# Performance work log

Measured on AMD Instinct MI355X. Metric: run time of the kernel, lower is better.

## Reference

```python
import jax, jax.numpy as jnp
import numpy as np

EPS = 1e-8  # matches F.cosine_similarity default eps
SIM_TARGET = 1  # int(self.sim_matrix), a scalar constant


def setup_inputs() -> dict:
    key = jax.random.key(0)
    k1, k2 = jax.random.split(key)
    input1 = jax.random.normal(k1, (4096, 1024), dtype=jnp.float32)  # [U, P]
    input2 = jax.random.normal(k2, (4096, 1024), dtype=jnp.float32)  # [V, P]
    return {"input1": input1, "input2": input2}


def reference(input1, input2):
    # Row-normalize with eps clamp (same as F.cosine_similarity per pair)
    n1 = input1 / jnp.maximum(jnp.linalg.norm(input1, axis=1, keepdims=True), EPS)
    n2 = input2 / jnp.maximum(jnp.linalg.norm(input2, axis=1, keepdims=True), EPS)
    cos = jnp.einsum('up,vp->uv', n1, n2)  # [U, V] pairwise cosine similarity
    return jnp.sum((SIM_TARGET - cos) ** 2)
```

## Files before the change

### kernel.cpp

```cpp
#include <hip/hip_runtime.h>
#include <hip/hip_bf16.h>
#include <stdint.h>

#define U_ROWS 4096
#define P_DIM  1024
#define TM     256
#define TN     128
#define BK     64

typedef float f32x4 __attribute__((ext_vector_type(4)));
typedef long  lx2   __attribute__((ext_vector_type(2)));

__global__ __launch_bounds__(256) void norm_fp8_kernel(
    const float* __restrict__ in1, const float* __restrict__ in2,
    uint8_t* __restrict__ out, float* __restrict__ loss_out) {
    const int w = threadIdx.x >> 6, lane = threadIdx.x & 63;
    const int row = blockIdx.x * 4 + w;
    const float* src = (row < U_ROWS) ? (in1 + (size_t)row * P_DIM)
                                      : (in2 + (size_t)(row - U_ROWS) * P_DIM);
    float4 v[4];
    float ss = 0.0f;
    #pragma unroll
    for (int j = 0; j < 4; ++j) {
        v[j] = ((const float4*)src)[j * 64 + lane];
        ss += v[j].x * v[j].x + v[j].y * v[j].y + v[j].z * v[j].z + v[j].w * v[j].w;
    }
    #pragma unroll
    for (int off = 32; off > 0; off >>= 1) ss += __shfl_xor(ss, off, 64);
    const float inv = 16.0f / fmaxf(sqrtf(ss), 1e-8f);

    uint8_t* orow = out + (size_t)row * P_DIM;
    #pragma unroll
    for (int j = 0; j < 4; ++j) {
        int c = j * 256 + lane * 4;
        int pos = (c & 4) + (((c >> 3) & 3) * 16) + (((c >> 5) & 1) * 8);
        int newc = (c & ~63) | pos;
        int d = __builtin_amdgcn_cvt_pk_fp8_f32(v[j].x * inv, v[j].y * inv, 0, false);
        d = __builtin_amdgcn_cvt_pk_fp8_f32(v[j].z * inv, v[j].w * inv, d, true);
        *(int*)(orow + newc) = d;
    }
    if (blockIdx.x == 0 && threadIdx.x == 0) *loss_out = 0.0f;
}

__global__ __launch_bounds__(512) void cosloss_gemm_fp8(
    const uint8_t* __restrict__ n1, const uint8_t* __restrict__ n2,
    float* __restrict__ loss_out) {
    __shared__ uint8_t As[TM * BK];
    __shared__ uint8_t Bs[TN * BK];
    __shared__ float red[8];

    const int tid  = threadIdx.x;
    const int w    = tid >> 6;
    const int lane = tid & 63;

    const int id  = blockIdx.x;
    const int xcd = id & 7;
    const int j   = id >> 3;
    const int cb  = xcd * 4 + (j & 3);
    const int rb  = j >> 2;

    const uint8_t* gA = n1 + (size_t)rb * TM * P_DIM;
    const uint8_t* gB = n2 + (size_t)cb * TN * P_DIM;

    const int srow = lane >> 2;
    const int scol = (lane & 3) * 16;
    const int chunk0 = w * 3;

    f32x4 acc[4][4];
    #pragma unroll
    for (int mi = 0; mi < 4; ++mi)
        #pragma unroll
        for (int ni = 0; ni < 4; ++ni)
            acc[mi][ni] = (f32x4){0.f, 0.f, 0.f, 0.f};

    const int wr = (w >> 1) * 64;
    const int wc = (w & 1) * 64;
    const int fr = lane & 15;
    const int q  = lane >> 4;

    for (int kt = 0; kt < P_DIM / BK; ++kt) {
        #pragma unroll
        for (int cc = 0; cc < 3; ++cc) {
            const int c = chunk0 + cc;
            const uint8_t* g;
            uint8_t* s;
            if (c < 16) {
                g = gA + (size_t)(c * 16 + srow) * P_DIM + kt * BK + scol;
                s = As + c * 1024;
            } else {
                g = gB + (size_t)((c - 16) * 16 + srow) * P_DIM + kt * BK + scol;
                s = Bs + (c - 16) * 1024;
            }
            __builtin_amdgcn_global_load_lds(
                (const __attribute__((address_space(1))) void*)g,
                (__attribute__((address_space(3))) void*)s,
                16, 0, 0);
        }
        __syncthreads();

        lx2 af[4], bfr[4];
        #pragma unroll
        for (int i = 0; i < 4; ++i) {
            af[i]  = *(const lx2*)(As + (wr + i * 16 + fr) * BK + q * 16);
            bfr[i] = *(const lx2*)(Bs + (wc + i * 16 + fr) * BK + q * 16);
        }
        #pragma unroll
        for (int mi = 0; mi < 4; ++mi)
            #pragma unroll
            for (int ni = 0; ni < 4; ++ni) {
                acc[mi][ni] = __builtin_amdgcn_mfma_f32_16x16x32_fp8_fp8(
                    af[mi].x, bfr[ni].x, acc[mi][ni], 0, 0, 0);
                acc[mi][ni] = __builtin_amdgcn_mfma_f32_16x16x32_fp8_fp8(
                    af[mi].y, bfr[ni].y, acc[mi][ni], 0, 0, 0);
            }
        __syncthreads();
    }

    float local = 0.0f;
    #pragma unroll
    for (int mi = 0; mi < 4; ++mi)
        #pragma unroll
        for (int ni = 0; ni < 4; ++ni)
            #pragma unroll
            for (int r = 0; r < 4; ++r) {
                const float d = 1.0f - acc[mi][ni][r] * (1.0f / 256.0f);
                local += d * d;
            }
    #pragma unroll
    for (int off = 32; off > 0; off >>= 1) local += __shfl_down(local, off, 64);
    if (lane == 0) red[w] = local;
    __syncthreads();
    if (tid == 0) {
        float t = 0.0f;
        #pragma unroll
        for (int i = 0; i < 8; ++i) t += red[i];
        atomicAdd(loss_out, t);
    }
}

extern "C" void kernel_launch(void* const* d_in, const int* in_sizes, int n_in,
                              void* d_out, int out_size, void* d_ws, size_t ws_size,
                              hipStream_t stream) {
    const float* in1 = (const float*)d_in[0];
    const float* in2 = (const float*)d_in[1];
    float* out = (float*)d_out;
    uint8_t* nrm = (uint8_t*)d_ws;

    norm_fp8_kernel<<<(U_ROWS * 2) / 4, 256, 0, stream>>>(in1, in2, nrm, out);

    cosloss_gemm_fp8<<<(U_ROWS / TM) * (U_ROWS / TN), 512, 0, stream>>>(
        nrm, nrm + (size_t)U_ROWS * P_DIM, out);
}
```

Baseline: 101.5 us.

## Switch FP8 GEMM to scaled 16x16x128 MFMA with swizzled K=128 tiles

Replaces the pairs of 16x16x32 fp8 MFMAs with the gfx950 scaled 16x16x128 f8f6f4 MFMA using unit scales, and doubles BK to 128 so each k-step issues one wide MFMA per tile. The normalization kernel now writes each row contiguously with a row-rotated 16-byte swizzle so the GEMM's LDS reads avoid bank conflicts. Launch bounds now request 4 blocks per CU. The aim is higher matrix throughput and fewer instructions and barriers, at the cost of a larger LDS footprint (48KB per block), which may limit occupancy.

```diff
diff --git a/kernel.cpp b/kernel.cpp
--- a/kernel.cpp
+++ b/kernel.cpp
@@ -6,10 +6,11 @@
 #define P_DIM  1024
 #define TM     256
 #define TN     128
-#define BK     64
+#define BK     128
 
 typedef float f32x4 __attribute__((ext_vector_type(4)));
-typedef long  lx2   __attribute__((ext_vector_type(2)));
+typedef int   i32x4 __attribute__((ext_vector_type(4)));
+typedef int   i32x8 __attribute__((ext_vector_type(8)));
 
 __global__ __launch_bounds__(256) void norm_fp8_kernel(
     const float* __restrict__ in1, const float* __restrict__ in2,
@@ -22,27 +23,28 @@
     float ss = 0.0f;
     #pragma unroll
     for (int j = 0; j < 4; ++j) {
-        v[j] = ((const float4*)src)[j * 64 + lane];
+        v[j] = ((const float4*)src)[lane * 4 + j];
         ss += v[j].x * v[j].x + v[j].y * v[j].y + v[j].z * v[j].z + v[j].w * v[j].w;
     }
     #pragma unroll
     for (int off = 32; off > 0; off >>= 1) ss += __shfl_xor(ss, off, 64);
     const float inv = 16.0f / fmaxf(sqrtf(ss), 1e-8f);
 
-    uint8_t* orow = out + (size_t)row * P_DIM;
+    i32x4 d;
     #pragma unroll
     for (int j = 0; j < 4; ++j) {
-        int c = j * 256 + lane * 4;
-        int pos = (c & 4) + (((c >> 3) & 3) * 16) + (((c >> 5) & 1) * 8);
-        int newc = (c & ~63) | pos;
-        int d = __builtin_amdgcn_cvt_pk_fp8_f32(v[j].x * inv, v[j].y * inv, 0, false);
-        d = __builtin_amdgcn_cvt_pk_fp8_f32(v[j].z * inv, v[j].w * inv, d, true);
-        *(int*)(orow + newc) = d;
+        int dj = __builtin_amdgcn_cvt_pk_fp8_f32(v[j].x * inv, v[j].y * inv, 0, false);
+        dj = __builtin_amdgcn_cvt_pk_fp8_f32(v[j].z * inv, v[j].w * inv, dj, true);
+        d[j] = dj;
     }
+    const int blk = lane >> 3;
+    const int gi  = lane & 7;
+    uint8_t* orow = out + (size_t)row * P_DIM;
+    *(i32x4*)(orow + blk * 128 + (((gi + row) & 7) * 16)) = d;
     if (blockIdx.x == 0 && threadIdx.x == 0) *loss_out = 0.0f;
 }
 
-__global__ __launch_bounds__(512) void cosloss_gemm_fp8(
+__global__ __launch_bounds__(512, 4) void cosloss_gemm_mx(
     const uint8_t* __restrict__ n1, const uint8_t* __restrict__ n2,
     float* __restrict__ loss_out) {
     __shared__ uint8_t As[TM * BK];
@@ -62,9 +64,9 @@
     const uint8_t* gA = n1 + (size_t)rb * TM * P_DIM;
     const uint8_t* gB = n2 + (size_t)cb * TN * P_DIM;
 
-    const int srow = lane >> 2;
-    const int scol = (lane & 3) * 16;
-    const int chunk0 = w * 3;
+    const int srow = lane >> 3;
+    const int scol = (lane & 7) * 16;
+    const int c0   = w * 6;
 
     f32x4 acc[4][4];
     #pragma unroll
@@ -80,16 +82,16 @@
 
     for (int kt = 0; kt < P_DIM / BK; ++kt) {
         #pragma unroll
-        for (int cc = 0; cc < 3; ++cc) {
-            const int c = chunk0 + cc;
+        for (int cc = 0; cc < 6; ++cc) {
+            const int c = c0 + cc;
             const uint8_t* g;
             uint8_t* s;
-            if (c < 16) {
-                g = gA + (size_t)(c * 16 + srow) * P_DIM + kt * BK + scol;
+            if (c < 32) {
+                g = gA + (size_t)(c * 8 + srow) * P_DIM + kt * BK + scol;
                 s = As + c * 1024;
             } else {
-                g = gB + (size_t)((c - 16) * 16 + srow) * P_DIM + kt * BK + scol;
-                s = Bs + (c - 16) * 1024;
+                g = gB + (size_t)((c - 32) * 8 + srow) * P_DIM + kt * BK + scol;
+                s = Bs + (c - 32) * 1024;
             }
             __builtin_amdgcn_global_load_lds(
                 (const __attribute__((address_space(1))) void*)g,
@@ -98,21 +100,30 @@
         }
         __syncthreads();
 
-        lx2 af[4], bfr[4];
+        i32x8 af[4];
         #pragma unroll
         for (int i = 0; i < 4; ++i) {
-            af[i]  = *(const lx2*)(As + (wr + i * 16 + fr) * BK + q * 16);
-            bfr[i] = *(const lx2*)(Bs + (wc + i * 16 + fr) * BK + q * 16);
+            const int row = wr + i * 16 + fr;
+            const uint8_t* rbase = As + row * BK;
+            i32x4 lo = *(const i32x4*)(rbase + (((q * 2 + 0 + row) & 7) * 16));
+            i32x4 hi = *(const i32x4*)(rbase + (((q * 2 + 1 + row) & 7) * 16));
+            af[i] = (i32x8){lo.x, lo.y, lo.z, lo.w, hi.x, hi.y, hi.z, hi.w};
         }
         #pragma unroll
-        for (int mi = 0; mi < 4; ++mi)
+        for (int ni = 0; ni < 4; ++ni) {
+            const int row = wc + ni * 16 + fr;
+            const uint8_t* rbase = Bs + row * BK;
+            i32x4 lo = *(const i32x4*)(rbase + (((q * 2 + 0 + row) & 7) * 16));
+            i32x4 hi = *(const i32x4*)(rbase + (((q * 2 + 1 + row) & 7) * 16));
+            i32x8 bf = (i32x8){lo.x, lo.y, lo.z, lo.w, hi.x, hi.y, hi.z, hi.w};
             #pragma unroll
-            for (int ni = 0; ni < 4; ++ni) {
-                acc[mi][ni] = __builtin_amdgcn_mfma_f32_16x16x32_fp8_fp8(
-                    af[mi].x, bfr[ni].x, acc[mi][ni], 0, 0, 0);
-                acc[mi][ni] = __builtin_amdgcn_mfma_f32_16x16x32_fp8_fp8(
-                    af[mi].y, bfr[ni].y, acc[mi][ni], 0, 0, 0);
-            }
+            for (int mi = 0; mi < 4; ++mi)
+                acc[mi][ni] = __builtin_amdgcn_mfma_scale_f32_16x16x128_f8f6f4(
+                    af[mi], bf, acc[mi][ni],
+                    0, 0,
+                    0, 0x7F,
+                    0, 0x7F);
+        }
         __syncthreads();
     }
 
@@ -123,8 +134,8 @@
         for (int ni = 0; ni < 4; ++ni)
             #pragma unroll
             for (int r = 0; r < 4; ++r) {
-                const float d = 1.0f - acc[mi][ni][r] * (1.0f / 256.0f);
-                local += d * d;
+                const float dd = 1.0f - acc[mi][ni][r] * (1.0f / 256.0f);
+                local += dd * dd;
             }
     #pragma unroll
     for (int off = 32; off > 0; off >>= 1) local += __shfl_down(local, off, 64);
@@ -148,6 +159,6 @@
 
     norm_fp8_kernel<<<(U_ROWS * 2) / 4, 256, 0, stream>>>(in1, in2, nrm, out);
 
-    cosloss_gemm_fp8<<<(U_ROWS / TM) * (U_ROWS / TN), 512, 0, stream>>>(
+    cosloss_gemm_mx<<<(U_ROWS / TM) * (U_ROWS / TN), 512, 0, stream>>>(
         nrm, nrm + (size_t)U_ROWS * P_DIM, out);
 }
```

New measurement: 304.2 us. +199.8%, slower.

## Switch cosine GEMM to int8 MFMA with double-buffered, swizzled LDS tiles

Applied to the files above, without the earlier changes.

Normalized rows are now quantized to int8 with a 512 scale instead of fp8, and the GEMM uses the 16x16x64 int8 MFMA with int32 accumulators, halving the MFMA instruction count per K-tile. LDS tiles are double-buffered so the next tile's global-to-LDS load is issued before the current tile's compute, which also drops one barrier per iteration. An XOR swizzle on the 16-byte column groups is meant to avoid LDS bank conflicts. The int8 quantization changes precision characteristics versus fp8 (uniform step, clamping at ±127), and the doubled LDS footprint may reduce occupancy.

```diff
diff --git a/kernel.cpp b/kernel.cpp
--- a/kernel.cpp
+++ b/kernel.cpp
@@ -8,12 +8,11 @@
 #define TN     128
 #define BK     64
 
-typedef float f32x4 __attribute__((ext_vector_type(4)));
-typedef long  lx2   __attribute__((ext_vector_type(2)));
+typedef int i32x4 __attribute__((ext_vector_type(4)));
 
-__global__ __launch_bounds__(256) void norm_fp8_kernel(
+__global__ __launch_bounds__(256) void norm_i8_kernel(
     const float* __restrict__ in1, const float* __restrict__ in2,
-    uint8_t* __restrict__ out, float* __restrict__ loss_out) {
+    int8_t* __restrict__ out, float* __restrict__ loss_out) {
     const int w = threadIdx.x >> 6, lane = threadIdx.x & 63;
     const int row = blockIdx.x * 4 + w;
     const float* src = (row < U_ROWS) ? (in1 + (size_t)row * P_DIM)
@@ -22,31 +21,31 @@
     float ss = 0.0f;
     #pragma unroll
     for (int j = 0; j < 4; ++j) {
-        v[j] = ((const float4*)src)[j * 64 + lane];
+        v[j] = ((const float4*)src)[lane * 4 + j];
         ss += v[j].x * v[j].x + v[j].y * v[j].y + v[j].z * v[j].z + v[j].w * v[j].w;
     }
     #pragma unroll
     for (int off = 32; off > 0; off >>= 1) ss += __shfl_xor(ss, off, 64);
-    const float inv = 16.0f / fmaxf(sqrtf(ss), 1e-8f);
+    const float inv = 512.0f / fmaxf(sqrtf(ss), 1e-8f);
 
-    uint8_t* orow = out + (size_t)row * P_DIM;
+    i32x4 d;
     #pragma unroll
     for (int j = 0; j < 4; ++j) {
-        int c = j * 256 + lane * 4;
-        int pos = (c & 4) + (((c >> 3) & 3) * 16) + (((c >> 5) & 1) * 8);
-        int newc = (c & ~63) | pos;
-        int d = __builtin_amdgcn_cvt_pk_fp8_f32(v[j].x * inv, v[j].y * inv, 0, false);
-        d = __builtin_amdgcn_cvt_pk_fp8_f32(v[j].z * inv, v[j].w * inv, d, true);
-        *(int*)(orow + newc) = d;
+        int q0 = max(-127, min(127, (int)rintf(v[j].x * inv)));
+        int q1 = max(-127, min(127, (int)rintf(v[j].y * inv)));
+        int q2 = max(-127, min(127, (int)rintf(v[j].z * inv)));
+        int q3 = max(-127, min(127, (int)rintf(v[j].w * inv)));
+        d[j] = (q0 & 255) | ((q1 & 255) << 8) | ((q2 & 255) << 16) | (q3 << 24);
     }
+    *(i32x4*)(out + (size_t)row * P_DIM + lane * 16) = d;
     if (blockIdx.x == 0 && threadIdx.x == 0) *loss_out = 0.0f;
 }
 
-__global__ __launch_bounds__(512) void cosloss_gemm_fp8(
-    const uint8_t* __restrict__ n1, const uint8_t* __restrict__ n2,
+__global__ __launch_bounds__(512) void cosloss_gemm_i8(
+    const int8_t* __restrict__ n1, const int8_t* __restrict__ n2,
     float* __restrict__ loss_out) {
-    __shared__ uint8_t As[TM * BK];
-    __shared__ uint8_t Bs[TN * BK];
+    __shared__ __align__(16) uint8_t As[2][TM * BK];
+    __shared__ __align__(16) uint8_t Bs[2][TN * BK];
     __shared__ float red[8];
 
     const int tid  = threadIdx.x;
@@ -59,61 +58,84 @@
     const int cb  = xcd * 4 + (j & 3);
     const int rb  = j >> 2;
 
-    const uint8_t* gA = n1 + (size_t)rb * TM * P_DIM;
-    const uint8_t* gB = n2 + (size_t)cb * TN * P_DIM;
+    const uint8_t* gA = (const uint8_t*)n1 + (size_t)rb * TM * P_DIM;
+    const uint8_t* gB = (const uint8_t*)n2 + (size_t)cb * TN * P_DIM;
 
     const int srow = lane >> 2;
-    const int scol = (lane & 3) * 16;
-    const int chunk0 = w * 3;
+    const int g    = lane & 3;
+    const int swc  = (g ^ (srow & 3)) * 16;
+    const int c0   = w * 3;
 
-    f32x4 acc[4][4];
+    i32x4 acc[4][4];
     #pragma unroll
     for (int mi = 0; mi < 4; ++mi)
         #pragma unroll
         for (int ni = 0; ni < 4; ++ni)
-            acc[mi][ni] = (f32x4){0.f, 0.f, 0.f, 0.f};
+            acc[mi][ni] = (i32x4){0, 0, 0, 0};
 
     const int wr = (w >> 1) * 64;
     const int wc = (w & 1) * 64;
     const int fr = lane & 15;
     const int q  = lane >> 4;
 
+    const int gsl = (q ^ (fr & 3)) * 16;
+    int aoff[4], boff[4];
+    #pragma unroll
+    for (int i = 0; i < 4; ++i) {
+        aoff[i] = (wr + i * 16 + fr) * BK + gsl;
+        boff[i] = (wc + i * 16 + fr) * BK + gsl;
+    }
+
+    #pragma unroll
+    for (int cc = 0; cc < 3; ++cc) {
+        const int c = c0 + cc;
+        const uint8_t* gsrc;
+        uint8_t* sdst;
+        if (c < 16) { gsrc = gA + (size_t)(c * 16 + srow) * P_DIM + swc;
+                      sdst = As[0] + c * 1024; }
+        else        { gsrc = gB + (size_t)((c - 16) * 16 + srow) * P_DIM + swc;
+                      sdst = Bs[0] + (c - 16) * 1024; }
+        __builtin_amdgcn_global_load_lds(
+            (const __attribute__((address_space(1))) void*)gsrc,
+            (__attribute__((address_space(3))) void*)sdst, 16, 0, 0);
+    }
+
+    #pragma unroll 2
     for (int kt = 0; kt < P_DIM / BK; ++kt) {
-        #pragma unroll
-        for (int cc = 0; cc < 3; ++cc) {
-            const int c = chunk0 + cc;
-            const uint8_t* g;
-            uint8_t* s;
-            if (c < 16) {
-                g = gA + (size_t)(c * 16 + srow) * P_DIM + kt * BK + scol;
-                s = As + c * 1024;
-            } else {
-                g = gB + (size_t)((c - 16) * 16 + srow) * P_DIM + kt * BK + scol;
-                s = Bs + (c - 16) * 1024;
-            }
-            __builtin_amdgcn_global_load_lds(
-                (const __attribute__((address_space(1))) void*)g,
-                (__attribute__((address_space(3))) void*)s,
-                16, 0, 0);
-        }
+        const int cur = kt & 1;
         __syncthreads();
 
-        lx2 af[4], bfr[4];
+        if (kt + 1 < P_DIM / BK) {
+            #pragma unroll
+            for (int cc = 0; cc < 3; ++cc) {
+                const int c = c0 + cc;
+                const uint8_t* gsrc;
+                uint8_t* sdst;
+                if (c < 16) {
+                    gsrc = gA + (size_t)(c * 16 + srow) * P_DIM + (kt + 1) * BK + swc;
+                    sdst = As[cur ^ 1] + c * 1024;
+                } else {
+                    gsrc = gB + (size_t)((c - 16) * 16 + srow) * P_DIM + (kt + 1) * BK + swc;
+                    sdst = Bs[cur ^ 1] + (c - 16) * 1024;
+                }
+                __builtin_amdgcn_global_load_lds(
+                    (const __attribute__((address_space(1))) void*)gsrc,
+                    (__attribute__((address_space(3))) void*)sdst, 16, 0, 0);
+            }
+        }
+
+        i32x4 af[4], bf[4];
         #pragma unroll
         for (int i = 0; i < 4; ++i) {
-            af[i]  = *(const lx2*)(As + (wr + i * 16 + fr) * BK + q * 16);
-            bfr[i] = *(const lx2*)(Bs + (wc + i * 16 + fr) * BK + q * 16);
+            af[i] = *(const i32x4*)(As[cur] + aoff[i]);
+            bf[i] = *(const i32x4*)(Bs[cur] + boff[i]);
         }
         #pragma unroll
         for (int mi = 0; mi < 4; ++mi)
             #pragma unroll
-            for (int ni = 0; ni < 4; ++ni) {
-                acc[mi][ni] = __builtin_amdgcn_mfma_f32_16x16x32_fp8_fp8(
-                    af[mi].x, bfr[ni].x, acc[mi][ni], 0, 0, 0);
-                acc[mi][ni] = __builtin_amdgcn_mfma_f32_16x16x32_fp8_fp8(
-                    af[mi].y, bfr[ni].y, acc[mi][ni], 0, 0, 0);
-            }
-        __syncthreads();
+            for (int ni = 0; ni < 4; ++ni)
+                acc[mi][ni] = __builtin_amdgcn_mfma_i32_16x16x64_i8(
+                    af[mi], bf[ni], acc[mi][ni], 0, 0, 0);
     }
 
     float local = 0.0f;
@@ -123,8 +145,8 @@
         for (int ni = 0; ni < 4; ++ni)
             #pragma unroll
             for (int r = 0; r < 4; ++r) {
-                const float d = 1.0f - acc[mi][ni][r] * (1.0f / 256.0f);
-                local += d * d;
+                const float dd = 1.0f - (float)acc[mi][ni][r] * (1.0f / 262144.0f);
+                local += dd * dd;
             }
     #pragma unroll
     for (int off = 32; off > 0; off >>= 1) local += __shfl_down(local, off, 64);
@@ -144,10 +166,10 @@
     const float* in1 = (const float*)d_in[0];
     const float* in2 = (const float*)d_in[1];
     float* out = (float*)d_out;
-    uint8_t* nrm = (uint8_t*)d_ws;
+    int8_t* nrm = (int8_t*)d_ws;
 
-    norm_fp8_kernel<<<(U_ROWS * 2) / 4, 256, 0, stream>>>(in1, in2, nrm, out);
+    norm_i8_kernel<<<(U_ROWS * 2) / 4, 256, 0, stream>>>(in1, in2, nrm, out);
 
-    cosloss_gemm_fp8<<<(U_ROWS / TM) * (U_ROWS / TN), 512, 0, stream>>>(
+    cosloss_gemm_i8<<<(U_ROWS / TM) * (U_ROWS / TN), 512, 0, stream>>>(
         nrm, nrm + (size_t)U_ROWS * P_DIM, out);
 }
```

Result: faster. 97.29 us (-4.1%).
